# Performance work log

Measured on AMD Instinct MI355X. Metric: run time of the kernel, lower is better.

## Reference

```python
import jax, jax.numpy as jnp
import numpy as np

EMB, HEADS, LAT, FFN = 1024, 16, 256, 4096
HD = EMB // HEADS
B, N = 2, 2048

def _ln(x, w, b, eps=1e-5):
    mu = jnp.mean(x, axis=-1, keepdims=True)
    var = jnp.var(x, axis=-1, keepdims=True)
    return (x - mu) * jax.lax.rsqrt(var + eps) * w + b

def setup_inputs() -> dict:
    key = jax.random.key(0)
    ks = jax.random.split(key, 16)
    def lin(k, fan_in, fan_out):
        bound = 1.0 / np.sqrt(fan_in)
        kw, kb = jax.random.split(k)
        W = jax.random.uniform(kw, (fan_in, fan_out), jnp.float32, -bound, bound)
        b = jax.random.uniform(kb, (fan_out,), jnp.float32, -bound, bound)
        return W, b
    Wq, bq = lin(ks[0], EMB, EMB)
    WaK, baK = lin(ks[1], EMB, LAT)
    WbK, bbK = lin(ks[2], LAT, EMB)
    WaV, baV = lin(ks[3], EMB, LAT)
    WbV, bbV = lin(ks[4], LAT, EMB)
    Wo, bo = lin(ks[5], EMB, EMB)
    W1, b1 = lin(ks[6], EMB, FFN)
    W2, b2 = lin(ks[7], FFN, EMB)
    return {
        'x': jax.random.normal(ks[8], (B, N, EMB), jnp.float32),
        'attn_bias': jax.random.normal(ks[9], (N, N), jnp.float32),
        'Wq': Wq, 'bq': bq, 'WaK': WaK, 'baK': baK, 'WbK': WbK, 'bbK': bbK,
        'WaV': WaV, 'baV': baV, 'WbV': WbV, 'bbV': bbV, 'Wo': Wo, 'bo': bo,
        'W1': W1, 'b1': b1, 'W2': W2, 'b2': b2,
        'ln1_w': jnp.ones((EMB,), jnp.float32), 'ln1_b': jnp.zeros((EMB,), jnp.float32),
        'ln2_w': jnp.ones((EMB,), jnp.float32), 'ln2_b': jnp.zeros((EMB,), jnp.float32),
    }

def reference(x, attn_bias, Wq, bq, WaK, baK, WbK, bbK, WaV, baV, WbV, bbV,
              Wo, bo, W1, b1, W2, b2, ln1_w, ln1_b, ln2_w, ln2_b):
    Q = x @ Wq + bq                       # [B,N,E]
    K = (x @ WaK + baK) @ WbK + bbK       # low-rank K
    V = (x @ WaV + baV) @ WbV + bbV       # low-rank V
    def split(t):
        return t.reshape(B, N, HEADS, HD).transpose(0, 2, 1, 3)  # [B,H,N,D]
    Qh, Kh, Vh = split(Q), split(K), split(V)
    scores = jnp.einsum('bhnd,bhmd->bhnm', Qh, Kh) / np.sqrt(HD)
    scores = scores + attn_bias[None, None]
    weights = jax.nn.softmax(scores, axis=-1)
    attn = jnp.einsum('bhnm,bhmd->bhnd', weights, Vh)
    attn = attn.transpose(0, 2, 1, 3).reshape(B, N, EMB)
    attn = attn @ Wo + bo
    h = _ln(x + attn, ln1_w, ln1_b)
    ffn = jax.nn.gelu(h @ W1 + b1, approximate=False) @ W2 + b2
    return _ln(h + ffn, ln2_w, ln2_b)
```

## Files before the change

kernel.cpp:

```cpp
#include <hip/hip_runtime.h>
#include <hip/hip_bf16.h>
#include <math.h>

typedef unsigned short u16;
typedef short bf16x8 __attribute__((ext_vector_type(8)));
typedef float f32x4 __attribute__((ext_vector_type(4)));

#define EMB   1024
#define HEADS 16
#define HD    64
#define LATD  256
#define FFND  4096
#define BATCH 2
#define SEQ   2048
#define TOK   (BATCH*SEQ)

#define SCL2  0.18033688011112042f
#define LOG2E 1.4426950408889634f

__device__ __forceinline__ float bf2f(u16 u) {
    union { unsigned int i; float f; } x; x.i = ((unsigned int)u) << 16; return x.f;
}
__device__ __forceinline__ u16 f2bf(float f) {
    union { float f; unsigned int i; } x; x.f = f;
    unsigned int i = x.i;
    unsigned int lsb = (i >> 16) & 1u;
    i += 0x7fffu + lsb;
    return (u16)(i >> 16);
}
__device__ __forceinline__ void gld16(const u16* g, u16* l) {
    __builtin_amdgcn_global_load_lds(
        (const __attribute__((address_space(1))) void*)g,
        (__attribute__((address_space(3))) void*)l, 16, 0, 0);
}
__device__ __forceinline__ unsigned int cvt_pk_bf16(float a, float b) {
    unsigned int r;
    asm("v_cvt_pk_bf16_f32 %0, %1, %2" : "=v"(r) : "v"(a), "v"(b));
    return r;
}
#if defined(__has_builtin)
#if __has_builtin(__builtin_amdgcn_exp2f)
#define EXP2(x) __builtin_amdgcn_exp2f(x)
#endif
#endif
#ifndef EXP2
#define EXP2(x) exp2f(x)
#endif

__global__ __launch_bounds__(256) void cvt_f32_bf16_kernel(
    const float* __restrict__ in, u16* __restrict__ out, int n8)
{
    int i = blockIdx.x * 256 + threadIdx.x;
    int stride = gridDim.x * 256;
    for (; i < n8; i += stride) {
        float4 f0 = *(const float4*)(in + (size_t)i * 8);
        float4 f1 = *(const float4*)(in + (size_t)i * 8 + 4);
        u16 e[8];
        e[0] = f2bf(f0.x); e[1] = f2bf(f0.y); e[2] = f2bf(f0.z); e[3] = f2bf(f0.w);
        e[4] = f2bf(f1.x); e[5] = f2bf(f1.y); e[6] = f2bf(f1.z); e[7] = f2bf(f1.w);
        *(uint4*)(out + (size_t)i * 8) = *(const uint4*)e;
    }
}

__global__ __launch_bounds__(256) void prep_bias_kernel(
    const float* __restrict__ a, const float* __restrict__ b,
    const float* __restrict__ q, float* __restrict__ bKV, float* __restrict__ bqs)
{
    int i = blockIdx.x * 256 + threadIdx.x;
    if (i < 256)      bKV[i] = a[i];
    else if (i < 512) bKV[i] = b[i - 256];
    else              bqs[i - 512] = q[i - 512] * SCL2;
}

__global__ __launch_bounds__(256) void permute_ab_kernel(
    const float* __restrict__ ab, float* __restrict__ abP)
{
    const int kt = blockIdx.x, qt = blockIdx.y;
    const int tid = threadIdx.x;
    const int lane = tid & 63, wq = tid >> 6;
    const int qq = lane >> 4, col = lane & 15;
#pragma unroll
    for (int wi = wq; wi < 8; wi += 4)
#pragma unroll
        for (int mt = 0; mt < 4; mt++) {
            float4 v = *(const float4*)(ab + (size_t)(qt * 128 + wi * 16 + col) * SEQ
                                        + kt * 64 + mt * 16 + qq * 4);
            v.x *= LOG2E; v.y *= LOG2E; v.z *= LOG2E; v.w *= LOG2E;
            *(float4*)(abP + (((size_t)qt * 32 + kt) * 8 + wi) * 1024 + mt * 256 + lane * 4) = v;
        }
}

struct TDesc { const float* src; u16* dst; int K; int N; int ofs; float scl; };
struct TTable { TDesc d[8]; };

__global__ __launch_bounds__(256) void transpose_all_kernel(TTable tt)
{
    __shared__ u16 t[32][33];
    int tb = blockIdx.x, e = 0;
#pragma unroll
    for (int i = 1; i < 8; i++) if (tb >= tt.d[i].ofs) e = i;
    const float* src = tt.d[e].src;
    u16* dst = tt.d[e].dst;
    const int K = tt.d[e].K, N = tt.d[e].N;
    const float scl = tt.d[e].scl;
    const int local = tb - tt.d[e].ofs;
    const int nx = N >> 5;
    const int bx = (local % nx) * 32;
    const int by = (local / nx) * 32;
    const int tx = threadIdx.x & 31;
    const int ty = threadIdx.x >> 5;
#pragma unroll
    for (int i = 0; i < 32; i += 8)
        t[ty + i][tx] = f2bf(src[(size_t)(by + ty + i) * N + bx + tx] * scl);
    __syncthreads();
#pragma unroll
    for (int i = 0; i < 32; i += 8)
        dst[(size_t)(bx + ty + i) * K + by + tx] = t[tx][ty + i];
}

#define BM 128
#define GBK 64

template <int ACT, int BNv, int TRC>
__device__ __forceinline__ void gemm_body(
    const u16* __restrict__ A, int lda, const u16* __restrict__ WT,
    const float* __restrict__ bias, u16* __restrict__ C,
    int K, int N, int bx, u16* Al, u16* Wl, u16* Tl)
{
    const int NT = BNv / 32;
    const int WN = BNv / 2;
    const int CW = BNv / 32;

    const int tid  = threadIdx.x;
    const int lane = tid & 63;
    const int w    = tid >> 6;
    const int wm = w >> 1, wn = w & 1;
    const int col = lane & 15, qq = lane >> 4;
    const size_t bm = (size_t)blockIdx.y * BM;
    const size_t bn = (size_t)bx * BNv;

    f32x4 acc[4][NT];
#pragma unroll
    for (int mt = 0; mt < 4; mt++)
#pragma unroll
        for (int nt = 0; nt < NT; nt++) acc[mt][nt] = (f32x4){0.f, 0.f, 0.f, 0.f};

    const u16* gA[4]; u16* lA[4];
#pragma unroll
    for (int i = 0; i < 4; i++) {
        int f = w * 256 + i * 64 + lane;
        int r = f >> 3, s = f & 7, sg = s ^ (r & 7);
        gA[i] = A + (bm + r) * (size_t)lda + sg * 8;
        lA[i] = &Al[(size_t)(w * 256 + i * 64) * 8];
    }
    const u16* gW[4]; u16* lW[4];
#pragma unroll
    for (int i = 0; i < CW; i++) {
        int f = w * (BNv * 2) + i * 64 + lane;
        int r = f >> 3, s = f & 7, sg = s ^ (r & 7);
        gW[i] = WT + (bn + r) * (size_t)K + sg * 8;
        lW[i] = &Wl[(size_t)(w * (BNv * 2) + i * 64) * 8];
    }

    for (int k0 = 0; k0 < K; k0 += GBK) {
#pragma unroll
        for (int i = 0; i < 4; i++) gld16(gA[i] + k0, lA[i]);
#pragma unroll
        for (int i = 0; i < CW; i++) gld16(gW[i] + k0, lW[i]);
        __syncthreads();

#pragma unroll
        for (int kk = 0; kk < 2; kk++) {
            bf16x8 af[4], bfr[NT];
#pragma unroll
            for (int mt = 0; mt < 4; mt++) {
                int rr = wm * 64 + mt * 16 + col;
                int sub = (kk * 4 + qq) ^ (rr & 7);
                af[mt] = *(const bf16x8*)&Al[rr * GBK + sub * 8];
            }
#pragma unroll
            for (int nt = 0; nt < NT; nt++) {
                int rn = wn * WN + nt * 16 + col;
                int sub = (kk * 4 + qq) ^ (rn & 7);
                bfr[nt] = *(const bf16x8*)&Wl[rn * GBK + sub * 8];
            }
#pragma unroll
            for (int mt = 0; mt < 4; mt++)
#pragma unroll
                for (int nt = 0; nt < NT; nt++)
                    acc[mt][nt] = __builtin_amdgcn_mfma_f32_16x16x32_bf16(
                        af[mt], bfr[nt], acc[mt][nt], 0, 0, 0);
        }
        __syncthreads();
    }

    float bv[NT];
#pragma unroll
    for (int nt = 0; nt < NT; nt++)
        bv[nt] = bias[bn + wn * WN + nt * 16 + col];

    if (TRC) {
#pragma unroll
        for (int mt = 0; mt < 4; mt++)
#pragma unroll
            for (int nt = 0; nt < NT; nt++)
#pragma unroll
                for (int r = 0; r < 4; r++) {
                    float v = acc[mt][nt][r] + bv[nt];
                    Tl[(wn * WN + nt * 16 + col) * 136 + (wm * 64 + mt * 16 + qq * 4 + r)] = f2bf(v);
                }
        __syncthreads();
        const int b_ = (int)(bm >> 11);
        const size_t tokb = bm & (SEQ - 1);
        const int row = tid >> 2;
        u16* dst = C + ((size_t)b_ * EMB + (size_t)bx * 64 + row) * SEQ + tokb;
        const u16* srcl = Tl + row * 136;
#pragma unroll
        for (int j = 0; j < 4; j++) {
            int c0 = ((tid & 3) + j * 4) * 8;
            *(uint4*)(dst + c0) = *(const uint4*)(srcl + c0);
        }
        return;
    }

#pragma unroll
    for (int mt = 0; mt < 4; mt++) {
#pragma unroll
        for (int nt = 0; nt < NT; nt++) {
#pragma unroll
            for (int r = 0; r < 4; r++) {
                float v = acc[mt][nt][r] + bv[nt];
                if (ACT == 1) v = 0.5f * v * (1.0f + erff(v * 0.70710678118654752f));
                size_t rg = bm + wm * 64 + mt * 16 + qq * 4 + r;
                C[rg * (size_t)N + bn + wn * WN + nt * 16 + col] = f2bf(v);
            }
        }
    }
}

template <int ACT, int BNv, int MINW>
__global__ __launch_bounds__(256, MINW) void gemm_bt_kernel(
    const u16* __restrict__ A, int lda, const u16* __restrict__ WT,
    const float* __restrict__ bias, u16* __restrict__ C,
    int K, int N)
{
    __shared__ __align__(16) u16 Al[BM * GBK];
    __shared__ __align__(16) u16 Wl[BNv * GBK];
    gemm_body<ACT, BNv, 0>(A, lda, WT, bias, C, K, N, blockIdx.x, Al, Wl, Al);
}

struct GPair {
    const u16* A0; const u16* A1;
    const u16* W0; const u16* W1;
    const float* b0; const float* b1;
    u16* C0; u16* C1;
    int lda0, lda1, N0, N1, nx0;
};

template <int BNv, int MINW, int TRV>
__global__ __launch_bounds__(256, MINW) void gemm_pair_kernel(GPair p, int K)
{
    __shared__ __align__(16) u16 SH[BM * GBK + BNv * GBK];
    u16* Al = SH;
    u16* Wl = SH + BM * GBK;
    const bool s1 = (int)blockIdx.x >= p.nx0;
    const u16* A = s1 ? p.A1 : p.A0;
    const u16* WT = s1 ? p.W1 : p.W0;
    const float* bias = s1 ? p.b1 : p.b0;
    u16* C = s1 ? p.C1 : p.C0;
    const int lda = s1 ? p.lda1 : p.lda0;
    const int N = s1 ? p.N1 : p.N0;
    const int bx = s1 ? (int)blockIdx.x - p.nx0 : (int)blockIdx.x;
    if (TRV && s1)
        gemm_body<0, BNv, 1>(A, lda, WT, bias, C, K, N, bx, Al, Wl, SH);
    else
        gemm_body<0, BNv, 0>(A, lda, WT, bias, C, K, N, bx, Al, Wl, SH);
}

#define BQ   128
#define BKV  64
#define NKVT (SEQ / BKV)
#define LDK  72
#define LDP  72
#define LDV  72

__global__ __launch_bounds__(512, 4) void fattn_kernel(
    const u16* __restrict__ Q, const u16* __restrict__ K,
    const u16* __restrict__ VT, const float* __restrict__ abP,
    u16* __restrict__ O)
{
    __shared__ __align__(16) u16 Ks[2][BKV * LDK];
    __shared__ __align__(16) u16 Vt[2][HD * LDV];
    __shared__ __align__(16) u16 Ps[BQ * LDP];

    const int tid = threadIdx.x;
    const int lane = tid & 63;
    const int w = tid >> 6;
    const int col = lane & 15, qq = lane >> 4;
    const int qt = blockIdx.x;
    const int b = blockIdx.y >> 4, h = blockIdx.y & 15;
    const size_t tok0 = (size_t)b * SEQ + (size_t)qt * BQ;
    const int wrow = w * 16;
    const size_t kvbase = (size_t)b * SEQ * EMB + h * HD;
    const size_t vtb = ((size_t)b * EMB + h * HD) * SEQ;

    const int krow = tid >> 3, kcol = (tid & 7) * 8;

    bf16x8 aq[2];
#pragma unroll
    for (int kk = 0; kk < 2; kk++)
        aq[kk] = *(const bf16x8*)(Q + (tok0 + wrow + col) * EMB + h * HD + kk * 32 + qq * 8);

    float m_st = -1e30f, l_st = 0.f;
    f32x4 o_acc[4];
#pragma unroll
    for (int dt = 0; dt < 4; dt++) o_acc[dt] = (f32x4){0.f, 0.f, 0.f, 0.f};

    uint4 kreg, vreg;
#define LOADKV(KV0) do {                                                              \
        kreg = *(const uint4*)(K + kvbase + (size_t)((KV0) + krow) * EMB + kcol);     \
        vreg = *(const uint4*)(VT + vtb + (size_t)krow * SEQ + (KV0) + kcol);         \
    } while (0)

    LOADKV(0);
    *(uint4*)&Ks[0][krow * LDK + kcol] = kreg;
    *(uint4*)&Vt[0][krow * LDV + kcol] = vreg;
    __syncthreads();
    LOADKV(BKV);

    const float* abq = abP + (size_t)qt * NKVT * 8192 + (size_t)w * 1024;
    f32x4 abv[4];
#pragma unroll
    for (int mt = 0; mt < 4; mt++)
        abv[mt] = *(const f32x4*)(abq + mt * 256 + lane * 4);

    for (int t = 0; t < NKVT; t++) {
        const int cur = t & 1;
        const u16* Kc = Ks[cur];

        f32x4 s2[4];
#pragma unroll
        for (int mt = 0; mt < 4; mt++) s2[mt] = abv[mt];
        __builtin_amdgcn_s_setprio(1);
#pragma unroll
        for (int mt = 0; mt < 4; mt++) {
            bf16x8 ak0 = *(const bf16x8*)&Kc[(mt * 16 + col) * LDK + qq * 8];
            bf16x8 ak1 = *(const bf16x8*)&Kc[(mt * 16 + col) * LDK + 32 + qq * 8];
            s2[mt] = __builtin_amdgcn_mfma_f32_16x16x32_bf16(ak0, aq[0], s2[mt], 0, 0, 0);
            s2[mt] = __builtin_amdgcn_mfma_f32_16x16x32_bf16(ak1, aq[1], s2[mt], 0, 0, 0);
        }
        __builtin_amdgcn_s_setprio(0);

        if (t + 1 < NKVT) {
            const float* abn = abq + (size_t)(t + 1) * 8192;
#pragma unroll
            for (int mt = 0; mt < 4; mt++)
                abv[mt] = *(const f32x4*)(abn + mt * 256 + lane * 4);
        }

        if (t + 1 < NKVT) {
            *(uint4*)&Ks[cur ^ 1][krow * LDK + kcol] = kreg;
            *(uint4*)&Vt[cur ^ 1][krow * LDV + kcol] = vreg;
        }
        if (t + 2 < NKVT) LOADKV((t + 2) * BKV);

        float t0 = fmaxf(fmaxf(s2[0][0], s2[0][1]), fmaxf(s2[0][2], s2[0][3]));
        float t1 = fmaxf(fmaxf(s2[1][0], s2[1][1]), fmaxf(s2[1][2], s2[1][3]));
        float t2 = fmaxf(fmaxf(s2[2][0], s2[2][1]), fmaxf(s2[2][2], s2[2][3]));
        float t3 = fmaxf(fmaxf(s2[3][0], s2[3][1]), fmaxf(s2[3][2], s2[3][3]));
        float tm = fmaxf(fmaxf(t0, t1), fmaxf(t2, t3));
        tm = fmaxf(tm, __shfl_xor(tm, 16));
        tm = fmaxf(tm, __shfl_xor(tm, 32));
        if (!__all(tm <= m_st + 8.f)) {
            float mnew = fmaxf(m_st, tm);
            float alpha = EXP2(m_st - mnew);
            m_st = mnew;
            l_st *= alpha;
            float af[4];
#pragma unroll
            for (int r = 0; r < 4; r++) af[r] = __shfl(alpha, qq * 20 + r);
#pragma unroll
            for (int dt = 0; dt < 4; dt++)
#pragma unroll
                for (int r = 0; r < 4; r++) o_acc[dt][r] *= af[r];
        }
        float rs = 0.f;
#pragma unroll
        for (int mt = 0; mt < 4; mt++)
#pragma unroll
            for (int r = 0; r < 4; r++) {
                float e = EXP2(s2[mt][r] - m_st);
                s2[mt][r] = e;
                rs += e;
            }
        rs += __shfl_xor(rs, 16);
        rs += __shfl_xor(rs, 32);
        l_st += rs;

#pragma unroll
        for (int mt = 0; mt < 4; mt++) {
            uint2 pp;
            pp.x = cvt_pk_bf16(s2[mt][0], s2[mt][1]);
            pp.y = cvt_pk_bf16(s2[mt][2], s2[mt][3]);
            *(uint2*)&Ps[(wrow + col) * LDP + mt * 16 + qq * 4] = pp;
        }

        __builtin_amdgcn_s_setprio(1);
#pragma unroll
        for (int kk = 0; kk < 2; kk++) {
            bf16x8 ap = *(const bf16x8*)&Ps[(wrow + col) * LDP + kk * 32 + qq * 8];
#pragma unroll
            for (int dt = 0; dt < 4; dt++) {
                bf16x8 bv = *(const bf16x8*)&Vt[cur][(dt * 16 + col) * LDV + kk * 32 + qq * 8];
                o_acc[dt] = __builtin_amdgcn_mfma_f32_16x16x32_bf16(ap, bv, o_acc[dt], 0, 0, 0);
            }
        }
        __builtin_amdgcn_s_setprio(0);
        __syncthreads();
    }
#undef LOADKV

    float lr[4];
#pragma unroll
    for (int r = 0; r < 4; r++) lr[r] = 1.0f / __shfl(l_st, qq * 20 + r);
#pragma unroll
    for (int r = 0; r < 4; r++)
#pragma unroll
        for (int dt = 0; dt < 4; dt++)
            O[(tok0 + wrow + qq * 4 + r) * EMB + h * HD + dt * 16 + col]
                = f2bf(o_acc[dt][r] * lr[r]);
}

template <int AF32, int OUTF32>
__global__ __launch_bounds__(256) void ln_kernel(
    const void* __restrict__ A, const u16* __restrict__ R,
    const float* __restrict__ w, const float* __restrict__ bb,
    void* __restrict__ out)
{
    __shared__ float r1[4], r2[4];
    const int tid = threadIdx.x;
    const size_t row = blockIdx.x;

    float v[4];
    float s = 0.0f, s2 = 0.0f;
#pragma unroll
    for (int i = 0; i < 4; i++) {
        int c = tid + i * 256;
        float a = AF32 ? ((const float*)A)[row * EMB + c]
                       : bf2f(((const u16*)A)[row * EMB + c]);
        float t = a + bf2f(R[row * EMB + c]);
        v[i] = t;
        s += t; s2 += t * t;
    }
#pragma unroll
    for (int o = 32; o > 0; o >>= 1) {
        s  += __shfl_down(s, o);
        s2 += __shfl_down(s2, o);
    }
    if ((tid & 63) == 0) { r1[tid >> 6] = s; r2[tid >> 6] = s2; }
    __syncthreads();
    s  = r1[0] + r1[1] + r1[2] + r1[3];
    s2 = r2[0] + r2[1] + r2[2] + r2[3];

    float mu = s * (1.0f / EMB);
    float var = s2 * (1.0f / EMB) - mu * mu;
    float rs = rsqrtf(var + 1e-5f);

#pragma unroll
    for (int i = 0; i < 4; i++) {
        int c = tid + i * 256;
        float y = (v[i] - mu) * rs * w[c] + bb[c];
        if (OUTF32) ((float*)out)[row * EMB + c] = y;
        else        ((u16*)out)[row * EMB + c] = f2bf(y);
    }
}

extern "C" void kernel_launch(void* const* d_in, const int* in_sizes, int n_in,
                              void* d_out, int out_size, void* d_ws, size_t ws_size,
                              hipStream_t stream)
{
    const float* x    = (const float*)d_in[0];
    const float* ab   = (const float*)d_in[1];
    const float* Wq   = (const float*)d_in[2];
    const float* bq   = (const float*)d_in[3];
    const float* WaK  = (const float*)d_in[4];
    const float* baK  = (const float*)d_in[5];
    const float* WbK  = (const float*)d_in[6];
    const float* bbK  = (const float*)d_in[7];
    const float* WaV  = (const float*)d_in[8];
    const float* baV  = (const float*)d_in[9];
    const float* WbV  = (const float*)d_in[10];
    const float* bbV  = (const float*)d_in[11];
    const float* Wo   = (const float*)d_in[12];
    const float* bo   = (const float*)d_in[13];
    const float* W1   = (const float*)d_in[14];
    const float* b1   = (const float*)d_in[15];
    const float* W2   = (const float*)d_in[16];
    const float* b2   = (const float*)d_in[17];
    const float* ln1w = (const float*)d_in[18];
    const float* ln1b = (const float*)d_in[19];
    const float* ln2w = (const float*)d_in[20];
    const float* ln2b = (const float*)d_in[21];

    u16* w = (u16*)d_ws;
    size_t o = 0;
    u16* WqT  = w + o; o += (size_t)EMB * EMB;
    u16* WaKT = w + o; o += (size_t)EMB * LATD;
    u16* WaVT = w + o; o += (size_t)EMB * LATD;
    u16* WbKT = w + o; o += (size_t)LATD * EMB;
    u16* WbVT = w + o; o += (size_t)LATD * EMB;
    u16* WoT  = w + o; o += (size_t)EMB * EMB;
    u16* W1T  = w + o; o += (size_t)EMB * FFND;
    u16* W2T  = w + o; o += (size_t)FFND * EMB;
    u16* Qb   = w + o; o += (size_t)TOK * EMB;
    u16* Kb   = w + o; o += (size_t)TOK * EMB;
    u16* Vb   = w + o; o += (size_t)TOK * EMB;
    u16* aOb  = w + o; o += (size_t)TOK * EMB;
    u16* projb= w + o; o += (size_t)TOK * EMB;
    u16* hb   = w + o; o += (size_t)TOK * EMB;
    u16* xb   = w + o; o += (size_t)TOK * EMB;
    float* bKV = (float*)(w + o); o += 1024;
    float* bqs = (float*)(w + o); o += 2048;
    float* abP = (float*)projb;
    u16* KVa = aOb;
    u16* f1  = Qb;
    u16* f2  = projb;

    dim3 blk(256);

    cvt_f32_bf16_kernel<<<dim3(2048), blk, 0, stream>>>(x, xb, TOK * EMB / 8);
    prep_bias_kernel<<<dim3(6), blk, 0, stream>>>(baK, baV, bq, bKV, bqs);
    permute_ab_kernel<<<dim3(32, 16), blk, 0, stream>>>(ab, abP);

    TTable tt;
    tt.d[0] = {Wq,  WqT,  EMB,  EMB,  0,    SCL2};
    tt.d[1] = {WaK, WaKT, EMB,  LATD, 1024, 1.0f};
    tt.d[2] = {WaV, WaVT, EMB,  LATD, 1280, 1.0f};
    tt.d[3] = {WbK, WbKT, LATD, EMB,  1536, 1.0f};
    tt.d[4] = {WbV, WbVT, LATD, EMB,  1792, 1.0f};
    tt.d[5] = {Wo,  WoT,  EMB,  EMB,  2048, 1.0f};
    tt.d[6] = {W1,  W1T,  EMB,  FFND, 3072, 1.0f};
    tt.d[7] = {W2,  W2T,  FFND, EMB,  7168, 1.0f};
    transpose_all_kernel<<<dim3(11264), blk, 0, stream>>>(tt);

    {
        GPair p;
        p.A0 = xb;  p.A1 = xb;
        p.W0 = WqT; p.W1 = WaKT;
        p.b0 = bqs; p.b1 = bKV;
        p.C0 = Qb;  p.C1 = KVa;
        p.lda0 = EMB; p.lda1 = EMB;
        p.N0 = EMB; p.N1 = 512; p.nx0 = 16;
        gemm_pair_kernel<64, 3, 0><<<dim3(24, TOK / BM), blk, 0, stream>>>(p, EMB);
    }
    {
        GPair p;
        p.A0 = KVa;  p.A1 = KVa + LATD;
        p.W0 = WbKT; p.W1 = WbVT;
        p.b0 = bbK;  p.b1 = bbV;
        p.C0 = Kb;   p.C1 = Vb;
        p.lda0 = 512; p.lda1 = 512;
        p.N0 = EMB; p.N1 = EMB; p.nx0 = 16;
        gemm_pair_kernel<64, 3, 1><<<dim3(32, TOK / BM), blk, 0, stream>>>(p, LATD);
    }

    fattn_kernel<<<dim3(SEQ / BQ, BATCH * HEADS), dim3(512), 0, stream>>>(Qb, Kb, Vb, abP, aOb);

    gemm_bt_kernel<0,64,3><<<dim3(EMB / 64, TOK / BM), blk, 0, stream>>>(aOb, EMB, WoT, bo, projb, EMB, EMB);

    ln_kernel<1,0><<<dim3(TOK), blk, 0, stream>>>(x, projb, ln1w, ln1b, hb);

    gemm_bt_kernel<1,128,2><<<dim3(FFND / 128, TOK / BM), blk, 0, stream>>>(hb, EMB, W1T, b1, f1, EMB, FFND);
    gemm_bt_kernel<0,64,3><<<dim3(EMB / 64, TOK / BM), blk, 0, stream>>>(f1, FFND, W2T, b2, f2, FFND, EMB);

    ln_kernel<0,1><<<dim3(TOK), blk, 0, stream>>>(hb, f2, ln2w, ln2b, (float*)d_out);
}
```

Baseline: 379.5 us.

## Process two query tiles per attention block to reuse K/V tiles

Each flash-attention block now handles two 128-row query tiles and shares every staged K/V tile between them, halving K/V global loads and barrier count per query row. The P·V MFMA operands are swapped so the accumulator layout lets each lane write output rows directly, which drops the alpha and l shuffles. The occupancy hint falls from 4 to 2 blocks per CU to make room for the extra registers, and the grid is half as large. Separately, the Q/KV-latent GEMM pair switches to a wider 128-column tile with a different stage count.

```diff
diff --git a/kernel.cpp b/kernel.cpp
--- a/kernel.cpp
+++ b/kernel.cpp
@@ -284,7 +284,7 @@
 #define LDP  72
 #define LDV  72
 
-__global__ __launch_bounds__(512, 4) void fattn_kernel(
+__global__ __launch_bounds__(512, 2) void fattn_kernel(
     const u16* __restrict__ Q, const u16* __restrict__ K,
     const u16* __restrict__ VT, const float* __restrict__ abP,
     u16* __restrict__ O)
@@ -297,24 +297,32 @@
     const int lane = tid & 63;
     const int w = tid >> 6;
     const int col = lane & 15, qq = lane >> 4;
-    const int qt = blockIdx.x;
+    const int qtp = blockIdx.x;
     const int b = blockIdx.y >> 4, h = blockIdx.y & 15;
-    const size_t tok0 = (size_t)b * SEQ + (size_t)qt * BQ;
     const int wrow = w * 16;
     const size_t kvbase = (size_t)b * SEQ * EMB + h * HD;
     const size_t vtb = ((size_t)b * EMB + h * HD) * SEQ;
 
+    size_t tok0[2];
+#pragma unroll
+    for (int j = 0; j < 2; j++)
+        tok0[j] = (size_t)b * SEQ + (size_t)(qtp * 2 + j) * BQ;
+
     const int krow = tid >> 3, kcol = (tid & 7) * 8;
 
-    bf16x8 aq[2];
-#pragma unroll
-    for (int kk = 0; kk < 2; kk++)
-        aq[kk] = *(const bf16x8*)(Q + (tok0 + wrow + col) * EMB + h * HD + kk * 32 + qq * 8);
-
-    float m_st = -1e30f, l_st = 0.f;
-    f32x4 o_acc[4];
-#pragma unroll
-    for (int dt = 0; dt < 4; dt++) o_acc[dt] = (f32x4){0.f, 0.f, 0.f, 0.f};
+    bf16x8 aq[2][2];
+#pragma unroll
+    for (int j = 0; j < 2; j++)
+#pragma unroll
+        for (int kk = 0; kk < 2; kk++)
+            aq[j][kk] = *(const bf16x8*)(Q + (tok0[j] + wrow + col) * EMB + h * HD + kk * 32 + qq * 8);
+
+    float m_st[2] = {-1e30f, -1e30f}, l_st[2] = {0.f, 0.f};
+    f32x4 o_acc[2][4];
+#pragma unroll
+    for (int j = 0; j < 2; j++)
+#pragma unroll
+        for (int dt = 0; dt < 4; dt++) o_acc[j][dt] = (f32x4){0.f, 0.f, 0.f, 0.f};
 
     uint4 kreg, vreg;
 #define LOADKV(KV0) do {                                                              \
@@ -328,34 +336,45 @@
     __syncthreads();
     LOADKV(BKV);
 
-    const float* abq = abP + (size_t)qt * NKVT * 8192 + (size_t)w * 1024;
-    f32x4 abv[4];
-#pragma unroll
-    for (int mt = 0; mt < 4; mt++)
-        abv[mt] = *(const f32x4*)(abq + mt * 256 + lane * 4);
+    const float* abq[2];
+#pragma unroll
+    for (int j = 0; j < 2; j++)
+        abq[j] = abP + (size_t)(qtp * 2 + j) * NKVT * 8192 + (size_t)w * 1024;
+    f32x4 abv[2][4];
+#pragma unroll
+    for (int j = 0; j < 2; j++)
+#pragma unroll
+        for (int mt = 0; mt < 4; mt++)
+            abv[j][mt] = *(const f32x4*)(abq[j] + mt * 256 + lane * 4);
 
     for (int t = 0; t < NKVT; t++) {
         const int cur = t & 1;
         const u16* Kc = Ks[cur];
 
-        f32x4 s2[4];
-#pragma unroll
-        for (int mt = 0; mt < 4; mt++) s2[mt] = abv[mt];
+        f32x4 s2[2][4];
+#pragma unroll
+        for (int j = 0; j < 2; j++)
+#pragma unroll
+            for (int mt = 0; mt < 4; mt++) s2[j][mt] = abv[j][mt];
         __builtin_amdgcn_s_setprio(1);
 #pragma unroll
         for (int mt = 0; mt < 4; mt++) {
             bf16x8 ak0 = *(const bf16x8*)&Kc[(mt * 16 + col) * LDK + qq * 8];
             bf16x8 ak1 = *(const bf16x8*)&Kc[(mt * 16 + col) * LDK + 32 + qq * 8];
-            s2[mt] = __builtin_amdgcn_mfma_f32_16x16x32_bf16(ak0, aq[0], s2[mt], 0, 0, 0);
-            s2[mt] = __builtin_amdgcn_mfma_f32_16x16x32_bf16(ak1, aq[1], s2[mt], 0, 0, 0);
+#pragma unroll
+            for (int j = 0; j < 2; j++) {
+                s2[j][mt] = __builtin_amdgcn_mfma_f32_16x16x32_bf16(ak0, aq[j][0], s2[j][mt], 0, 0, 0);
+                s2[j][mt] = __builtin_amdgcn_mfma_f32_16x16x32_bf16(ak1, aq[j][1], s2[j][mt], 0, 0, 0);
+            }
         }
         __builtin_amdgcn_s_setprio(0);
 
         if (t + 1 < NKVT) {
-            const float* abn = abq + (size_t)(t + 1) * 8192;
-#pragma unroll
-            for (int mt = 0; mt < 4; mt++)
-                abv[mt] = *(const f32x4*)(abn + mt * 256 + lane * 4);
+#pragma unroll
+            for (int j = 0; j < 2; j++)
+#pragma unroll
+                for (int mt = 0; mt < 4; mt++)
+                    abv[j][mt] = *(const f32x4*)(abq[j] + (size_t)(t + 1) * 8192 + mt * 256 + lane * 4);
         }
 
         if (t + 1 < NKVT) {
@@ -364,71 +383,73 @@
         }
         if (t + 2 < NKVT) LOADKV((t + 2) * BKV);
 
-        float t0 = fmaxf(fmaxf(s2[0][0], s2[0][1]), fmaxf(s2[0][2], s2[0][3]));
-        float t1 = fmaxf(fmaxf(s2[1][0], s2[1][1]), fmaxf(s2[1][2], s2[1][3]));
-        float t2 = fmaxf(fmaxf(s2[2][0], s2[2][1]), fmaxf(s2[2][2], s2[2][3]));
-        float t3 = fmaxf(fmaxf(s2[3][0], s2[3][1]), fmaxf(s2[3][2], s2[3][3]));
-        float tm = fmaxf(fmaxf(t0, t1), fmaxf(t2, t3));
-        tm = fmaxf(tm, __shfl_xor(tm, 16));
-        tm = fmaxf(tm, __shfl_xor(tm, 32));
-        if (!__all(tm <= m_st + 8.f)) {
-            float mnew = fmaxf(m_st, tm);
-            float alpha = EXP2(m_st - mnew);
-            m_st = mnew;
-            l_st *= alpha;
-            float af[4];
-#pragma unroll
-            for (int r = 0; r < 4; r++) af[r] = __shfl(alpha, qq * 20 + r);
-#pragma unroll
-            for (int dt = 0; dt < 4; dt++)
-#pragma unroll
-                for (int r = 0; r < 4; r++) o_acc[dt][r] *= af[r];
-        }
-        float rs = 0.f;
-#pragma unroll
-        for (int mt = 0; mt < 4; mt++)
-#pragma unroll
-            for (int r = 0; r < 4; r++) {
-                float e = EXP2(s2[mt][r] - m_st);
-                s2[mt][r] = e;
-                rs += e;
-            }
-        rs += __shfl_xor(rs, 16);
-        rs += __shfl_xor(rs, 32);
-        l_st += rs;
-
-#pragma unroll
-        for (int mt = 0; mt < 4; mt++) {
+#pragma unroll
+        for (int j = 0; j < 2; j++) {
+            float t0 = fmaxf(fmaxf(s2[j][0][0], s2[j][0][1]), fmaxf(s2[j][0][2], s2[j][0][3]));
+            float t1 = fmaxf(fmaxf(s2[j][1][0], s2[j][1][1]), fmaxf(s2[j][1][2], s2[j][1][3]));
+            float t2 = fmaxf(fmaxf(s2[j][2][0], s2[j][2][1]), fmaxf(s2[j][2][2], s2[j][2][3]));
+            float t3 = fmaxf(fmaxf(s2[j][3][0], s2[j][3][1]), fmaxf(s2[j][3][2], s2[j][3][3]));
+            float tm = fmaxf(fmaxf(t0, t1), fmaxf(t2, t3));
+            tm = fmaxf(tm, __shfl_xor(tm, 16));
+            tm = fmaxf(tm, __shfl_xor(tm, 32));
+            if (!__all(tm <= m_st[j] + 8.f)) {
+                float mnew = fmaxf(m_st[j], tm);
+                float alpha = EXP2(m_st[j] - mnew);
+                m_st[j] = mnew;
+                l_st[j] *= alpha;
+#pragma unroll
+                for (int dt = 0; dt < 4; dt++)
+#pragma unroll
+                    for (int r = 0; r < 4; r++) o_acc[j][dt][r] *= alpha;
+            }
+            float rs = 0.f;
+#pragma unroll
+            for (int mt = 0; mt < 4; mt++)
+#pragma unroll
+                for (int r = 0; r < 4; r++) {
+                    float e = EXP2(s2[j][mt][r] - m_st[j]);
+                    s2[j][mt][r] = e;
+                    rs += e;
+                }
+            rs += __shfl_xor(rs, 16);
+            rs += __shfl_xor(rs, 32);
+            l_st[j] += rs;
+
+#pragma unroll
+            for (int mt = 0; mt < 4; mt++) {
+                uint2 pp;
+                pp.x = cvt_pk_bf16(s2[j][mt][0], s2[j][mt][1]);
+                pp.y = cvt_pk_bf16(s2[j][mt][2], s2[j][mt][3]);
+                *(uint2*)&Ps[(wrow + col) * LDP + mt * 16 + qq * 4] = pp;
+            }
+
+            __builtin_amdgcn_s_setprio(1);
+#pragma unroll
+            for (int kk = 0; kk < 2; kk++) {
+                bf16x8 ap = *(const bf16x8*)&Ps[(wrow + col) * LDP + kk * 32 + qq * 8];
+#pragma unroll
+                for (int dt = 0; dt < 4; dt++) {
+                    bf16x8 bv = *(const bf16x8*)&Vt[cur][(dt * 16 + col) * LDV + kk * 32 + qq * 8];
+                    o_acc[j][dt] = __builtin_amdgcn_mfma_f32_16x16x32_bf16(bv, ap, o_acc[j][dt], 0, 0, 0);
+                }
+            }
+            __builtin_amdgcn_s_setprio(0);
+        }
+        __syncthreads();
+    }
+#undef LOADKV
+
+#pragma unroll
+    for (int j = 0; j < 2; j++) {
+        float lr = 1.0f / l_st[j];
+#pragma unroll
+        for (int dt = 0; dt < 4; dt++) {
             uint2 pp;
-            pp.x = cvt_pk_bf16(s2[mt][0], s2[mt][1]);
-            pp.y = cvt_pk_bf16(s2[mt][2], s2[mt][3]);
-            *(uint2*)&Ps[(wrow + col) * LDP + mt * 16 + qq * 4] = pp;
-        }
-
-        __builtin_amdgcn_s_setprio(1);
-#pragma unroll
-        for (int kk = 0; kk < 2; kk++) {
-            bf16x8 ap = *(const bf16x8*)&Ps[(wrow + col) * LDP + kk * 32 + qq * 8];
-#pragma unroll
-            for (int dt = 0; dt < 4; dt++) {
-                bf16x8 bv = *(const bf16x8*)&Vt[cur][(dt * 16 + col) * LDV + kk * 32 + qq * 8];
-                o_acc[dt] = __builtin_amdgcn_mfma_f32_16x16x32_bf16(ap, bv, o_acc[dt], 0, 0, 0);
-            }
-        }
-        __builtin_amdgcn_s_setprio(0);
-        __syncthreads();
-    }
-#undef LOADKV
-
-    float lr[4];
-#pragma unroll
-    for (int r = 0; r < 4; r++) lr[r] = 1.0f / __shfl(l_st, qq * 20 + r);
-#pragma unroll
-    for (int r = 0; r < 4; r++)
-#pragma unroll
-        for (int dt = 0; dt < 4; dt++)
-            O[(tok0 + wrow + qq * 4 + r) * EMB + h * HD + dt * 16 + col]
-                = f2bf(o_acc[dt][r] * lr[r]);
+            pp.x = cvt_pk_bf16(o_acc[j][dt][0] * lr, o_acc[j][dt][1] * lr);
+            pp.y = cvt_pk_bf16(o_acc[j][dt][2] * lr, o_acc[j][dt][3] * lr);
+            *(uint2*)(O + (tok0[j] + wrow + col) * EMB + h * HD + dt * 16 + qq * 4) = pp;
+        }
+    }
 }
 
 template <int AF32, int OUTF32>
@@ -550,8 +571,8 @@
         p.b0 = bqs; p.b1 = bKV;
         p.C0 = Qb;  p.C1 = KVa;
         p.lda0 = EMB; p.lda1 = EMB;
-        p.N0 = EMB; p.N1 = 512; p.nx0 = 16;
-        gemm_pair_kernel<64, 3, 0><<<dim3(24, TOK / BM), blk, 0, stream>>>(p, EMB);
+        p.N0 = EMB; p.N1 = 512; p.nx0 = 8;
+        gemm_pair_kernel<128, 2, 0><<<dim3(12, TOK / BM), blk, 0, stream>>>(p, EMB);
     }
     {
         GPair p;
@@ -564,7 +585,7 @@
         gemm_pair_kernel<64, 3, 1><<<dim3(32, TOK / BM), blk, 0, stream>>>(p, LATD);
     }
 
-    fattn_kernel<<<dim3(SEQ / BQ, BATCH * HEADS), dim3(512), 0, stream>>>(Qb, Kb, Vb, abP, aOb);
+    fattn_kernel<<<dim3(SEQ / (2 * BQ), BATCH * HEADS), dim3(512), 0, stream>>>(Qb, Kb, Vb, abP, aOb);
 
     gemm_bt_kernel<0,64,3><<<dim3(EMB / 64, TOK / BM), blk, 0, stream>>>(aOb, EMB, WoT, bo, projb, EMB, EMB);
 
```

Result: slower. 395.5 us (+4.2%).
